# Optimization experiments

Measured on AMD Instinct MI355X. Metric: run time of the kernel, lower is better.

Reference implementation:

```python
import jax, jax.numpy as jnp
import numpy as np

B, S = 2, 2048
DIM_IN, DIM_OUT, NUM_HEADS, DIM_QK = 1024, 128, 16, 128


def setup_inputs() -> dict:
    key = jax.random.key(0)
    k0, k1, k2, k3 = jax.random.split(key, 4)
    x = jax.random.normal(k0, (B, S, DIM_IN), jnp.float32)
    mask = jax.random.bernoulli(k1, 0.1, (B, S))  # True = masked-out token
    # xavier-normal-ish scales (exact init values are irrelevant for correctness)
    std_in = float(np.sqrt(2.0 / (NUM_HEADS * DIM_QK + DIM_IN * DIM_QK)))
    proj_in = jax.random.normal(k2, (DIM_IN, NUM_HEADS, 2 * DIM_QK + DIM_OUT), jnp.float32) * std_in
    v_bias = jnp.zeros((NUM_HEADS, DIM_OUT), jnp.float32)
    std_out = float(np.sqrt(2.0 / (DIM_OUT * DIM_OUT + NUM_HEADS * DIM_OUT)))
    proj_out = jax.random.normal(k3, (NUM_HEADS, DIM_OUT, DIM_OUT), jnp.float32) * std_out
    proj_out_bias = jnp.zeros((DIM_OUT,), jnp.float32)
    return {"x": x, "mask": mask, "proj_in": proj_in, "v_bias": v_bias,
            "proj_out": proj_out, "proj_out_bias": proj_out_bias}


def _rotary(t):
    # t: [z, s, h, d]; GPT-NeoX style rotary as in the torch Rotary module
    d = t.shape[-1]
    half = -(-d // 2)  # ceil(d/2), matches torch.arange(0,-1,-2/d)
    freq_half = 10000.0 ** (jnp.arange(half, dtype=jnp.float32) * (-2.0 / d))
    freq = jnp.concatenate([freq_half, freq_half[: half - d % 2]])  # length d
    pos = jnp.arange(t.shape[1], dtype=jnp.float32)
    ang = pos[:, None] * freq[None, :]             # [s, d]
    cos = jnp.cos(ang)[None, :, None, :]
    sin = jnp.sin(ang)[None, :, None, :]
    x1, x2 = jnp.split(t, 2, axis=-1)
    rot = jnp.concatenate([-x2, x1], axis=-1)
    return t * cos + rot * sin


def _inf_cube(t):
    return t ** 3


def reference(x, mask, proj_in, v_bias, proj_out, proj_out_bias):
    qkv = jnp.einsum('zki,iho->zkho', x, proj_in)
    q, k, v = jnp.split(qkv, [DIM_QK, 2 * DIM_QK], axis=-1)
    q = _rotary(q)
    k = _rotary(k)
    scores = jnp.einsum('zqha,zkha->zqkh', q, k) / jnp.sqrt(jnp.float32(DIM_QK))
    # dual mask: row (query) OR column (key) masked -> -inf
    m = jnp.logical_or(mask[:, :, None, None], mask[:, None, :, None])  # [z,q,k,1]
    scores = jnp.where(m, -jnp.inf, scores)
    attn = jnp.nan_to_num(jax.nn.softmax(scores, axis=2))  # softmax over k; nan rows -> 0
    o = jnp.einsum('zqkh,zkhx->zqhx', attn, v + v_bias[None, None])
    out = jnp.einsum('zqhx,hxy->zqy', _inf_cube(o), proj_out) + proj_out_bias[None, None]
    return _inf_cube(out)
```

## Files before the change

kernel.cpp:

```cpp
#include <hip/hip_runtime.h>
#include <math.h>

#define BZ 2
#define SQ 2048
#define DIN 1024
#define HH 16
#define NT 6144
#define MROWS 4096
#define KOUT 2048
#define KSPLIT 8

typedef unsigned short u16t;
typedef unsigned int u32t;
typedef __attribute__((ext_vector_type(8))) short bf16x8;
typedef __attribute__((ext_vector_type(4))) float f32x4;

__device__ __forceinline__ float cubef(float x) { return x * x * x; }

__device__ __forceinline__ u16t f2bf(float f) {
    u32t b = __float_as_uint(f);
    b += 0x7FFFu + ((b >> 16) & 1u);
    return (u16t)(b >> 16);
}
__device__ __forceinline__ float bf2f(u16t u) { return __uint_as_float(((u32t)u) << 16); }
__device__ __forceinline__ u32t pk2(float a, float b) {
    return (u32t)f2bf(a) | ((u32t)f2bf(b) << 16);
}

#if __has_builtin(__builtin_amdgcn_exp2f)
#define EXP2(x) __builtin_amdgcn_exp2f(x)
#else
#define EXP2(x) exp2f(x)
#endif

__device__ __forceinline__ void load_lds16(const void* g, void* l) {
    __builtin_amdgcn_global_load_lds((const __attribute__((address_space(1))) void*)g,
                                     (__attribute__((address_space(3))) void*)l, 16, 0, 0);
}

__global__ __launch_bounds__(256) void prep_all(const float* __restrict__ x,
                                                u16t* __restrict__ xb,
                                                float* __restrict__ tab,
                                                const float* __restrict__ W,
                                                u16t* __restrict__ Th) {
    __shared__ float tile[64][68];
    const int bx = blockIdx.x;
    const int t = threadIdx.x;

    if (bx < 2048) {
        const size_t idx = ((size_t)bx * 256 + t) * 8;
        float4 f0 = *(const float4*)&x[idx];
        float4 f1 = *(const float4*)&x[idx + 4];
        u32t h[4];
        h[0] = pk2(f0.x, f0.y); h[1] = pk2(f0.z, f0.w);
        h[2] = pk2(f1.x, f1.y); h[3] = pk2(f1.z, f1.w);
        *(uint4*)&xb[idx] = *(uint4*)&h[0];
    } else if (bx < 2560) {
        const int idx = (bx - 2048) * 256 + t;
        const int s = idx >> 6, d = idx & 63;
        float f = expf(-0.14391156831212788f * (float)d);
        float sn, cs;
        sincosf((float)s * f, &sn, &cs);
        ((float2*)tab)[idx] = make_float2(cs, sn);
    } else {
        const int idx = bx - 2560;
        const int n0 = (idx % 96) * 64;
        const int k0 = (idx / 96) * 64;
        {
            const int r = t >> 4, c = (t & 15) * 4;
            #pragma unroll
            for (int p = 0; p < 4; p++) {
                float4 v = *(const float4*)&W[(size_t)(k0 + r + p * 16) * NT + n0 + c];
                *(float4*)&tile[r + p * 16][c] = v;
            }
        }
        __syncthreads();
        const int nr = t >> 2;
        const int kc = (t & 3) * 16;
        u32t hi[8];
        #pragma unroll
        for (int j = 0; j < 8; j++)
            hi[j] = pk2(tile[kc + 2 * j][nr], tile[kc + 2 * j + 1][nr]);
        size_t ob = (size_t)(n0 + nr) * DIN + k0 + kc;
        *(uint4*)&Th[ob]     = *(uint4*)&hi[0];
        *(uint4*)&Th[ob + 8] = *(uint4*)&hi[4];
    }
}

__global__ __launch_bounds__(256) void transpose_w2(const float* __restrict__ W,
                                                    u16t* __restrict__ Th) {
    __shared__ float tile[64][68];
    const int n0 = blockIdx.x * 64;
    const int k0 = blockIdx.y * 64;
    const int t = threadIdx.x;
    {
        const int r = t >> 4, c = (t & 15) * 4;
        #pragma unroll
        for (int p = 0; p < 4; p++) {
            float4 v = *(const float4*)&W[(size_t)(k0 + r + p * 16) * 128 + n0 + c];
            *(float4*)&tile[r + p * 16][c] = v;
        }
    }
    __syncthreads();
    const int nr = t >> 2;
    const int kc = (t & 3) * 16;
    u32t hi[8];
    #pragma unroll
    for (int j = 0; j < 8; j++)
        hi[j] = pk2(tile[kc + 2 * j][nr], tile[kc + 2 * j + 1][nr]);
    size_t ob = (size_t)(n0 + nr) * KOUT + k0 + kc;
    *(uint4*)&Th[ob]     = *(uint4*)&hi[0];
    *(uint4*)&Th[ob + 8] = *(uint4*)&hi[4];
}

#define QSC 0.12751744f

__global__ __launch_bounds__(256) void gemm_qkv11(const u16t* __restrict__ Ah,
                                                  const u16t* __restrict__ Bh,
                                                  const float* __restrict__ vb,
                                                  const float* __restrict__ ropetab,
                                                  u16t* __restrict__ QB,
                                                  u16t* __restrict__ KB,
                                                  u16t* __restrict__ VTh) {
    __shared__ __align__(16) u16t smem[17408];

    const int t = threadIdx.x;
    const int lane = t & 63, wid = t >> 6;
    const int quad = lane >> 4, l15 = lane & 15;
    const int wm = (wid & 1) * 64;
    const int wn = (wid >> 1) * 64;

    const int f = blockIdx.y * 48 + blockIdx.x;
    const int L = (f & 7) * 192 + (f >> 3);
    const int rect = L / 48, rrem = L - rect * 48;
    const int tileI = (rect & 7) * 6 + rrem % 6;
    const int rowIdx = (rect >> 3) * 8 + rrem / 6;
    const int h = tileI / 3, t3 = tileI - h * 3;
    const int colBase = tileI * 128;
    const int rowBase = rowIdx * 128;
    const int sm = t & 127;
    const int skh = t >> 7;

    f32x4 acc[4][4];
    #pragma unroll
    for (int i = 0; i < 4; i++)
        #pragma unroll
        for (int j = 0; j < 4; j++) acc[i][j] = (f32x4){0.f, 0.f, 0.f, 0.f};

    const u16t* aPtr = Ah + (size_t)(rowBase + sm) * DIN + skh * 16;
    const u16t* bPtr = Bh + (size_t)(colBase + sm) * DIN + skh * 16;
    const int swoff = skh * 2048 + sm * 8;

    uint4 a0 = *(const uint4*)(aPtr);
    uint4 a1 = *(const uint4*)(aPtr + 8);
    uint4 b0 = *(const uint4*)(bPtr);
    uint4 b1 = *(const uint4*)(bPtr + 8);

    for (int it = 0; it < 32; it++) {
        const int buf = it & 1;
        const int ab = buf * 4096, bb_ = 8192 + buf * 4096;
        *(uint4*)(&smem[ab + swoff])         = a0;
        *(uint4*)(&smem[ab + swoff + 1024])  = a1;
        *(uint4*)(&smem[bb_ + swoff])        = b0;
        *(uint4*)(&smem[bb_ + swoff + 1024]) = b1;
        __syncthreads();
        {
            const int k0 = (it < 31) ? (it + 1) * 32 : it * 32;
            a0 = *(const uint4*)(aPtr + k0);
            a1 = *(const uint4*)(aPtr + k0 + 8);
            b0 = *(const uint4*)(bPtr + k0);
            b1 = *(const uint4*)(bPtr + k0 + 8);
        }
        bf16x8 ah[4], bh[4];
        #pragma unroll
        for (int mt = 0; mt < 4; mt++)
            ah[mt] = *(const bf16x8*)&smem[ab + quad * 1024 + (wm + mt * 16 + l15) * 8];
        #pragma unroll
        for (int nt = 0; nt < 4; nt++)
            bh[nt] = *(const bf16x8*)&smem[bb_ + quad * 1024 + (wn + nt * 16 + l15) * 8];
        #pragma unroll
        for (int mt = 0; mt < 4; mt++)
            #pragma unroll
            for (int nt = 0; nt < 4; nt++)
                acc[mt][nt] = __builtin_amdgcn_mfma_f32_16x16x32_bf16(ah[mt], bh[nt], acc[mt][nt], 0, 0, 0);
    }
    __syncthreads();

    const int z = rowBase >> 11;
    const int s0local = rowBase & 2047;
    const size_t zh = (size_t)(z * 16 + h);
    u16t* tl = smem;

    if (t3 == 2) {
        #pragma unroll
        for (int nt = 0; nt < 4; nt++) {
            float bbv = vb[h * 128 + wn + nt * 16 + l15];
            #pragma unroll
            for (int mt = 0; mt < 4; mt++)
                #pragma unroll
                for (int r = 0; r < 4; r++)
                    tl[(wm + mt * 16 + quad * 4 + r) * 136 + wn + nt * 16 + l15] =
                        f2bf(acc[mt][nt][r] + bbv);
        }
    } else {
        #pragma unroll
        for (int nt = 0; nt < 4; nt++)
            #pragma unroll
            for (int mt = 0; mt < 4; mt++)
                #pragma unroll
                for (int r = 0; r < 4; r++)
                    tl[(wm + mt * 16 + quad * 4 + r) * 136 + wn + nt * 16 + l15] =
                        f2bf(acc[mt][nt][r]);
    }
    __syncthreads();

    if (t3 != 2) {
        u16t* dstQK = (t3 ? KB : QB) + zh * 262144;
        const float sc = t3 ? 1.0f : QSC;
        const int rr = t >> 2;
        const int ch = (t & 3) << 4;
        #pragma unroll
        for (int half = 0; half < 2; half++) {
            const int row = rr + half * 64;
            const int s = s0local + row;
            const u16t* trow = &tl[row * 136];
            uint4 X1  = *(const uint4*)&trow[ch];
            uint4 X1b = *(const uint4*)&trow[ch + 8];
            uint4 X2  = *(const uint4*)&trow[ch + 64];
            uint4 X2b = *(const uint4*)&trow[ch + 72];
            u32t A_[8] = {X1.x, X1.y, X1.z, X1.w, X1b.x, X1b.y, X1b.z, X1b.w};
            u32t B_[8] = {X2.x, X2.y, X2.z, X2.w, X2b.x, X2b.y, X2b.z, X2b.w};
            u32t OA[8], OB[8];
            const float4* tb = (const float4*)&ropetab[(size_t)s * 128 + ch * 2];
            #pragma unroll
            for (int p = 0; p < 8; p++) {
                float4 tt = tb[p];
                float cs0 = tt.x * sc, sn0 = tt.y * sc;
                float cs1 = tt.z * sc, sn1 = tt.w * sc;
                float x1a = bf2f((u16t)(A_[p] & 0xFFFFu)), x1b = bf2f((u16t)(A_[p] >> 16));
                float x2a = bf2f((u16t)(B_[p] & 0xFFFFu)), x2b = bf2f((u16t)(B_[p] >> 16));
                OA[p] = pk2(x1a * cs0 - x2a * sn0, x1b * cs1 - x2b * sn1);
                OB[p] = pk2(x2a * cs0 + x1a * sn0, x2b * cs1 + x1b * sn1);
            }
            u16t* d0 = dstQK + (size_t)s * 128 + ch;
            *(uint4*)d0        = make_uint4(OA[0], OA[1], OA[2], OA[3]);
            *(uint4*)(d0 + 8)  = make_uint4(OA[4], OA[5], OA[6], OA[7]);
            *(uint4*)(d0 + 64) = make_uint4(OB[0], OB[1], OB[2], OB[3]);
            *(uint4*)(d0 + 72) = make_uint4(OB[4], OB[5], OB[6], OB[7]);
        }
    } else {
        u16t* dstV = VTh + zh * 262144 + (size_t)(s0local >> 5) * 4096;
        const int d = t & 127;
        const int g0 = t >> 7;
        #pragma unroll
        for (int gg = 0; gg < 2; gg++) {
            const int g = g0 + 2 * gg;
            const u16t* col = &tl[(g * 32) * 136 + d];
            u32t H[16];
            #pragma unroll
            for (int m = 0; m < 16; m++) {
                u32t lo = col[m * 136];
                u32t hi = col[(m + 16) * 136];
                H[m] = lo | (hi << 16);
            }
            u16t* dv = dstV + (size_t)g * 4096 + d * 32;
            *(uint4*)&dv[0]  = *(uint4*)&H[0];
            *(uint4*)&dv[8]  = *(uint4*)&H[4];
            *(uint4*)&dv[16] = *(uint4*)&H[8];
            *(uint4*)&dv[24] = *(uint4*)&H[12];
        }
    }
}

__global__ __launch_bounds__(256, 2) void attn_kernel13(const u16t* __restrict__ QB,
                                                        const u16t* __restrict__ KB,
                                                        const u16t* __restrict__ VTh,
                                                        const int* __restrict__ mask,
                                                        u16t* __restrict__ O3b) {
    const int blk = blockIdx.x;
    const int xcd = blk & 7, loc = blk >> 3;
    const int zhl = xcd * 4 + (loc >> 4);
    const int qt = loc & 15;
    const int z = zhl >> 4, h = zhl & 15;
    const int t  = threadIdx.x;
    const int lane = t & 63, wid = t >> 6;
    const int quad = lane >> 4, l15 = lane & 15;

    __shared__ __align__(16) u16t ks[2][32 * 136];
    __shared__ __align__(16) u16t vth[2][128 * 40];
    __shared__ __align__(16) u16t wlb[128 * 40];

    const int q0 = qt * 128;
    const u16t* qb  = QB  + (size_t)zhl * 262144;
    const u16t* kb  = KB  + (size_t)zhl * 262144;
    const u16t* vhg = VTh + (size_t)zhl * 262144;
    const int mb = z * SQ;

    bf16x8 qf[2][4];
    #pragma unroll
    for (int i = 0; i < 2; i++)
        #pragma unroll
        for (int kk = 0; kk < 4; kk++)
            qf[i][kk] = *(const bf16x8*)(qb + (size_t)(q0 + 16 * (2 * wid + i) + l15) * 128 + kk * 32 + quad * 8);

    int4 qm4[2];
    #pragma unroll
    for (int i = 0; i < 2; i++)
        qm4[i] = *(const int4*)&mask[mb + q0 + 16 * (2 * wid + i) + 4 * quad];
    const int qmr[2][4] = {{qm4[0].x, qm4[0].y, qm4[0].z, qm4[0].w},
                           {qm4[1].x, qm4[1].y, qm4[1].z, qm4[1].w}};
    int rowoff[2];
    #pragma unroll
    for (int i = 0; i < 2; i++) rowoff[i] = (16 * (2 * wid + i) + 4 * quad) * 40;

    const int srow = t >> 3, sco = (t & 7) * 16;
    const int sdd = t >> 1, sk0 = (t & 1) * 16;

    uint4 ka, kb2, va, vb2;
    {
        ka  = *(const uint4*)(kb + t * 16);
        kb2 = *(const uint4*)(kb + t * 16 + 8);
        va  = *(const uint4*)(vhg + t * 16);
        vb2 = *(const uint4*)(vhg + t * 16 + 8);
    }

    f32x4 acc[2][8];
    #pragma unroll
    for (int i = 0; i < 2; i++)
        #pragma unroll
        for (int d = 0; d < 8; d++) acc[i][d] = (f32x4){0.f, 0.f, 0.f, 0.f};
    float dsum[2][4] = {{0.f, 0.f, 0.f, 0.f}, {0.f, 0.f, 0.f, 0.f}};

    for (int it = 0; it < 64; it++) {
        const int buf = it & 1;
        *(uint4*)&ks[buf][srow * 136 + sco]     = ka;
        *(uint4*)&ks[buf][srow * 136 + sco + 8] = kb2;
        *(uint4*)&vth[buf][sdd * 40 + sk0]      = va;
        *(uint4*)&vth[buf][sdd * 40 + sk0 + 8]  = vb2;

        __syncthreads();

        {
            const int ktn = (it < 63) ? (it + 1) * 32 : it * 32;
            const u16t* src = kb + (size_t)ktn * 128 + t * 16;
            ka  = *(const uint4*)(src);
            kb2 = *(const uint4*)(src + 8);
            const u16t* srch = vhg + (size_t)(ktn >> 5) * 4096 + t * 16;
            va  = *(const uint4*)(srch);
            vb2 = *(const uint4*)(srch + 8);
        }

        const int colm0 = mask[mb + it * 32 + l15];
        const int colm1 = mask[mb + it * 32 + 16 + l15];

        f32x4 s4[2][2];
        #pragma unroll
        for (int i = 0; i < 2; i++)
            #pragma unroll
            for (int n = 0; n < 2; n++) s4[i][n] = (f32x4){0.f, 0.f, 0.f, 0.f};
        __builtin_amdgcn_s_setprio(1);
        #pragma unroll
        for (int kk = 0; kk < 4; kk++) {
            bf16x8 kf0 = *(const bf16x8*)&ks[buf][l15 * 136 + kk * 32 + quad * 8];
            bf16x8 kf1 = *(const bf16x8*)&ks[buf][(16 + l15) * 136 + kk * 32 + quad * 8];
            s4[0][0] = __builtin_amdgcn_mfma_f32_16x16x32_bf16(qf[0][kk], kf0, s4[0][0], 0, 0, 0);
            s4[0][1] = __builtin_amdgcn_mfma_f32_16x16x32_bf16(qf[0][kk], kf1, s4[0][1], 0, 0, 0);
            s4[1][0] = __builtin_amdgcn_mfma_f32_16x16x32_bf16(qf[1][kk], kf0, s4[1][0], 0, 0, 0);
            s4[1][1] = __builtin_amdgcn_mfma_f32_16x16x32_bf16(qf[1][kk], kf1, s4[1][1], 0, 0, 0);
        }
        __builtin_amdgcn_s_setprio(0);
        {
            #pragma unroll
            for (int i = 0; i < 2; i++)
                #pragma unroll
                for (int r = 0; r < 4; r++) {
                    float w0 = colm0 ? 0.f : EXP2(s4[i][0][r]);
                    float w1 = colm1 ? 0.f : EXP2(s4[i][1][r]);
                    dsum[i][r] += w0 + w1;
                    u32t pkw;
                    asm("v_cvt_pk_bf16_f32 %0, %1, %2" : "=v"(pkw) : "v"(w0), "v"(w1));
                    *(u32t*)&wlb[rowoff[i] + r * 40 + 2 * l15] = pkw;
                }
        }
        bf16x8 pa[2];
        #pragma unroll
        for (int i = 0; i < 2; i++)
            pa[i] = *(const bf16x8*)&wlb[(16 * (2 * wid + i) + l15) * 40 + quad * 8];
        __builtin_amdgcn_s_setprio(1);
        #pragma unroll
        for (int dt = 0; dt < 8; dt++) {
            bf16x8 vh = *(const bf16x8*)&vth[buf][(16 * dt + l15) * 40 + quad * 8];
            acc[0][dt] = __builtin_amdgcn_mfma_f32_16x16x32_bf16(pa[0], vh, acc[0][dt], 0, 0, 0);
            acc[1][dt] = __builtin_amdgcn_mfma_f32_16x16x32_bf16(pa[1], vh, acc[1][dt], 0, 0, 0);
        }
        __builtin_amdgcn_s_setprio(0);
    }

    #pragma unroll
    for (int i = 0; i < 2; i++)
        #pragma unroll
        for (int r = 0; r < 4; r++) {
            float v = dsum[i][r];
            v += __shfl_xor(v, 1);
            v += __shfl_xor(v, 2);
            v += __shfl_xor(v, 4);
            v += __shfl_xor(v, 8);
            dsum[i][r] = v;
        }

    #pragma unroll
    for (int i = 0; i < 2; i++)
        #pragma unroll
        for (int r = 0; r < 4; r++) {
            int row = 16 * (2 * wid + i) + 4 * quad + r;
            float inv = (qmr[i][r] || !(dsum[i][r] > 0.f)) ? 0.f : 1.f / dsum[i][r];
            u16t* dst = O3b + (size_t)(z * SQ + q0 + row) * KOUT + h * 128;
            #pragma unroll
            for (int dt = 0; dt < 8; dt++)
                dst[16 * dt + l15] = f2bf(cubef(acc[i][dt][r] * inv));
        }
}

#define GQ_WAITBAR(N) do {                                                 \
    asm volatile("s_waitcnt vmcnt(" #N ")" ::: "memory");                  \
    __builtin_amdgcn_s_barrier();                                          \
    __builtin_amdgcn_sched_barrier(0);                                     \
} while (0)

#define GQ_STAGE(TI) do {                                                  \
    const int _k0 = (TI) * 32;                                             \
    const int _bb = ((TI) & 3) * 8192;                                     \
    load_lds16(aPtr + _k0,     &smem[_bb + wbase]);                        \
    load_lds16(aPtr + _k0 + 8, &smem[_bb + wbase + 1024]);                 \
    load_lds16(bPtr + _k0,     &smem[_bb + 4096 + wbase]);                 \
    load_lds16(bPtr + _k0 + 8, &smem[_bb + 4096 + wbase + 1024]);          \
} while (0)

#define GQ_COMPUTE(TI) do {                                                \
    const int _bb = ((TI) & 3) * 8192;                                     \
    bf16x8 ah[4], bh[4];                                                   \
    _Pragma("unroll")                                                      \
    for (int mt = 0; mt < 4; mt++)                                         \
        ah[mt] = *(const bf16x8*)&smem[_bb + quad * 1024 + (wm + mt * 16 + l15) * 8]; \
    _Pragma("unroll")                                                      \
    for (int nt = 0; nt < 4; nt++)                                         \
        bh[nt] = *(const bf16x8*)&smem[_bb + 4096 + quad * 1024 + (wn + nt * 16 + l15) * 8]; \
    _Pragma("unroll")                                                      \
    for (int mt = 0; mt < 4; mt++)                                         \
        _Pragma("unroll")                                                  \
        for (int nt = 0; nt < 4; nt++)                                     \
            acc[mt][nt] = __builtin_amdgcn_mfma_f32_16x16x32_bf16(ah[mt], bh[nt], acc[mt][nt], 0, 0, 0); \
} while (0)

__global__ __launch_bounds__(256, 2) void final_gemm4(const u16t* __restrict__ Ab,
                                                      const u16t* __restrict__ Bh,
                                                      float* __restrict__ part) {
    __shared__ __align__(16) u16t smem[32768];

    const int t = threadIdx.x;
    const int lane = t & 63, wid = t >> 6;
    const int quad = lane >> 4, l15 = lane & 15;
    const int wm = (wid & 1) * 64;
    const int wn = (wid >> 1) * 64;
    const int rowBase = blockIdx.x * 128;
    const int kBase   = blockIdx.y * (KOUT / KSPLIT);
    const int sm = t & 127;
    const int skh = t >> 7;

    f32x4 acc[4][4];
    #pragma unroll
    for (int i = 0; i < 4; i++)
        #pragma unroll
        for (int j = 0; j < 4; j++) acc[i][j] = (f32x4){0.f, 0.f, 0.f, 0.f};

    const u16t* aPtr = Ab + (size_t)(rowBase + sm) * KOUT + kBase + skh * 16;
    const u16t* bPtr = Bh + (size_t)sm * KOUT + kBase + skh * 16;
    const int wbase = (wid >> 1) * 2048 + (wid & 1) * 512;

    GQ_STAGE(0);
    GQ_STAGE(1);
    for (int i = 0; i < 6; i++) {
        GQ_STAGE(i + 2);
        GQ_WAITBAR(8);
        GQ_COMPUTE(i);
    }
    GQ_WAITBAR(4);
    GQ_COMPUTE(6);
    GQ_WAITBAR(0);
    GQ_COMPUTE(7);

    float* pbase = part + (size_t)blockIdx.y * ((size_t)MROWS * 128);
    #pragma unroll
    for (int mt = 0; mt < 4; mt++)
        #pragma unroll
        for (int nt = 0; nt < 4; nt++) {
            int col = wn + nt * 16 + l15;
            #pragma unroll
            for (int r = 0; r < 4; r++) {
                int row = rowBase + wm + mt * 16 + quad * 4 + r;
                pbase[(size_t)row * 128 + col] = acc[mt][nt][r];
            }
        }
}

__global__ __launch_bounds__(256) void reduce_bias_cube(const float* __restrict__ part,
                                                        const float* __restrict__ bias,
                                                        float* __restrict__ out) {
    const int idx = (blockIdx.x * 256 + threadIdx.x) * 4;
    float4 s = {0.f, 0.f, 0.f, 0.f};
    #pragma unroll
    for (int p = 0; p < KSPLIT; p++) {
        float4 v = *(const float4*)&part[(size_t)p * ((size_t)MROWS * 128) + idx];
        s.x += v.x; s.y += v.y; s.z += v.z; s.w += v.w;
    }
    float4 b = *(const float4*)&bias[idx & 127];
    float4 r;
    r.x = cubef(s.x + b.x);
    r.y = cubef(s.y + b.y);
    r.z = cubef(s.z + b.z);
    r.w = cubef(s.w + b.w);
    *(float4*)&out[idx] = r;
}

extern "C" void kernel_launch(void* const* d_in, const int* in_sizes, int n_in,
                              void* d_out, int out_size, void* d_ws, size_t ws_size,
                              hipStream_t stream) {
    const float* x        = (const float*)d_in[0];
    const int*   mask     = (const int*)d_in[1];
    const float* proj_in  = (const float*)d_in[2];
    const float* v_bias   = (const float*)d_in[3];
    const float* proj_out = (const float*)d_in[4];
    const float* po_bias  = (const float*)d_in[5];
    float* out = (float*)d_out;

    u16t* QB  = (u16t*)d_ws;
    u16t* KB  = QB + (size_t)8388608;
    u16t* VTh = KB + (size_t)8388608;
    u16t* xb  = VTh + (size_t)8388608;
    u16t* O3b = xb + (size_t)4194304;
    u16t* pTh = O3b;
    float* ropetab = (float*)(O3b + (size_t)6291456);
    u16t* WTh = QB;
    float* partials = (float*)(WTh + (size_t)128 * KOUT);

    prep_all<<<2048 + 512 + 1536, 256, 0, stream>>>(x, xb, ropetab, proj_in, pTh);
    gemm_qkv11<<<dim3(48, 32), 256, 0, stream>>>(xb, pTh, v_bias, ropetab, QB, KB, VTh);
    attn_kernel13<<<BZ * HH * (SQ / 128), 256, 0, stream>>>(QB, KB, VTh, mask, O3b);
    transpose_w2<<<dim3(2, KOUT / 64), 256, 0, stream>>>(proj_out, WTh);
    final_gemm4<<<dim3(MROWS / 128, KSPLIT), 256, 0, stream>>>(O3b, WTh, partials);
    reduce_bias_cube<<<(MROWS * 128) / (256 * 4), 256, 0, stream>>>(partials, po_bias, out);
}
```

Measured before the change: 295.2 us.

## Pipeline QKV GEMM with triple-buffered direct global-to-LDS loads

Replaces the register-staged double-buffered main loop of the QKV projection GEMM with a three-stage pipeline that uses direct global-to-LDS loads (load_lds16), vmcnt waits and one barrier per iteration. Two k-tiles are kept in flight while the current one is computed, which hides global load latency and drops the register round trip for staging. The cost is more LDS (48KB), which may lower occupancy. Correctness depends on the wbase layout matching what the compute reads and on each thread's async loads landing in order.

```diff
diff --git a/kernel.cpp b/kernel.cpp
--- a/kernel.cpp
+++ b/kernel.cpp
@@ -115,14 +115,45 @@
 
 #define QSC 0.12751744f
 
-__global__ __launch_bounds__(256) void gemm_qkv11(const u16t* __restrict__ Ah,
+#define GQ3_WAITBAR(N) do {                                                \
+    asm volatile("s_waitcnt vmcnt(" #N ")" ::: "memory");                  \
+    __builtin_amdgcn_s_barrier();                                          \
+    __builtin_amdgcn_sched_barrier(0);                                     \
+} while (0)
+
+#define GQ3_STAGE(TI) do {                                                 \
+    const int _k0 = (TI) * 32;                                             \
+    const int _bb = ((TI) % 3) * 8192;                                     \
+    load_lds16(aPtr + _k0,     &smem[_bb + wbase]);                        \
+    load_lds16(aPtr + _k0 + 8, &smem[_bb + wbase + 1024]);                 \
+    load_lds16(bPtr + _k0,     &smem[_bb + 4096 + wbase]);                 \
+    load_lds16(bPtr + _k0 + 8, &smem[_bb + 4096 + wbase + 1024]);          \
+} while (0)
+
+#define GQ3_COMPUTE(TI) do {                                               \
+    const int _bb = ((TI) % 3) * 8192;                                     \
+    bf16x8 ah[4], bh[4];                                                   \
+    _Pragma("unroll")                                                      \
+    for (int mt = 0; mt < 4; mt++)                                         \
+        ah[mt] = *(const bf16x8*)&smem[_bb + quad * 1024 + (wm + mt * 16 + l15) * 8]; \
+    _Pragma("unroll")                                                      \
+    for (int nt = 0; nt < 4; nt++)                                         \
+        bh[nt] = *(const bf16x8*)&smem[_bb + 4096 + quad * 1024 + (wn + nt * 16 + l15) * 8]; \
+    _Pragma("unroll")                                                      \
+    for (int mt = 0; mt < 4; mt++)                                         \
+        _Pragma("unroll")                                                  \
+        for (int nt = 0; nt < 4; nt++)                                     \
+            acc[mt][nt] = __builtin_amdgcn_mfma_f32_16x16x32_bf16(ah[mt], bh[nt], acc[mt][nt], 0, 0, 0); \
+} while (0)
+
+__global__ __launch_bounds__(256) void gemm_qkv12(const u16t* __restrict__ Ah,
                                                   const u16t* __restrict__ Bh,
                                                   const float* __restrict__ vb,
                                                   const float* __restrict__ ropetab,
                                                   u16t* __restrict__ QB,
                                                   u16t* __restrict__ KB,
                                                   u16t* __restrict__ VTh) {
-    __shared__ __align__(16) u16t smem[17408];
+    __shared__ __align__(16) u16t smem[24576];
 
     const int t = threadIdx.x;
     const int lane = t & 63, wid = t >> 6;
@@ -149,41 +180,19 @@
 
     const u16t* aPtr = Ah + (size_t)(rowBase + sm) * DIN + skh * 16;
     const u16t* bPtr = Bh + (size_t)(colBase + sm) * DIN + skh * 16;
-    const int swoff = skh * 2048 + sm * 8;
-
-    uint4 a0 = *(const uint4*)(aPtr);
-    uint4 a1 = *(const uint4*)(aPtr + 8);
-    uint4 b0 = *(const uint4*)(bPtr);
-    uint4 b1 = *(const uint4*)(bPtr + 8);
-
-    for (int it = 0; it < 32; it++) {
-        const int buf = it & 1;
-        const int ab = buf * 4096, bb_ = 8192 + buf * 4096;
-        *(uint4*)(&smem[ab + swoff])         = a0;
-        *(uint4*)(&smem[ab + swoff + 1024])  = a1;
-        *(uint4*)(&smem[bb_ + swoff])        = b0;
-        *(uint4*)(&smem[bb_ + swoff + 1024]) = b1;
-        __syncthreads();
-        {
-            const int k0 = (it < 31) ? (it + 1) * 32 : it * 32;
-            a0 = *(const uint4*)(aPtr + k0);
-            a1 = *(const uint4*)(aPtr + k0 + 8);
-            b0 = *(const uint4*)(bPtr + k0);
-            b1 = *(const uint4*)(bPtr + k0 + 8);
-        }
-        bf16x8 ah[4], bh[4];
-        #pragma unroll
-        for (int mt = 0; mt < 4; mt++)
-            ah[mt] = *(const bf16x8*)&smem[ab + quad * 1024 + (wm + mt * 16 + l15) * 8];
-        #pragma unroll
-        for (int nt = 0; nt < 4; nt++)
-            bh[nt] = *(const bf16x8*)&smem[bb_ + quad * 1024 + (wn + nt * 16 + l15) * 8];
-        #pragma unroll
-        for (int mt = 0; mt < 4; mt++)
-            #pragma unroll
-            for (int nt = 0; nt < 4; nt++)
-                acc[mt][nt] = __builtin_amdgcn_mfma_f32_16x16x32_bf16(ah[mt], bh[nt], acc[mt][nt], 0, 0, 0);
-    }
+    const int wbase = (wid >> 1) * 2048 + (wid & 1) * 512;
+
+    GQ3_STAGE(0);
+    GQ3_STAGE(1);
+    for (int i = 0; i < 30; i++) {
+        GQ3_WAITBAR(4);
+        GQ3_STAGE(i + 2);
+        GQ3_COMPUTE(i);
+    }
+    GQ3_WAITBAR(4);
+    GQ3_COMPUTE(30);
+    GQ3_WAITBAR(0);
+    GQ3_COMPUTE(31);
     __syncthreads();
 
     const int z = rowBase >> 11;
@@ -544,7 +553,7 @@
     float* partials = (float*)(WTh + (size_t)128 * KOUT);
 
     prep_all<<<2048 + 512 + 1536, 256, 0, stream>>>(x, xb, ropetab, proj_in, pTh);
-    gemm_qkv11<<<dim3(48, 32), 256, 0, stream>>>(xb, pTh, v_bias, ropetab, QB, KB, VTh);
+    gemm_qkv12<<<dim3(48, 32), 256, 0, stream>>>(xb, pTh, v_bias, ropetab, QB, KB, VTh);
     attn_kernel13<<<BZ * HH * (SQ / 128), 256, 0, stream>>>(QB, KB, VTh, mask, O3b);
     transpose_w2<<<dim3(2, KOUT / 64), 256, 0, stream>>>(proj_out, WTh);
     final_gemm4<<<dim3(MROWS / 128, KSPLIT), 256, 0, stream>>>(O3b, WTh, partials);
```

After: 298.7 us, median of 2. About the same (+1.2%).

## Pipeline QKV GEMM with direct-to-LDS loads in a 4-stage ring buffer

Applied to the files above, without the earlier changes.

Replaces the QKV projection GEMM's register-staged double buffer with direct global-to-LDS loads into a 4-slot ring, prefetching two K-steps ahead with vmcnt-based waits and one barrier per step. It also raises MFMA wave priority during compute through the shared macros and sets launch bounds to two blocks per CU. The aim is to hide global load latency and cut per-iteration synchronisation. In exchange LDS use grows to 64KB per block, which may limit occupancy, and the fixed wait counts must match the issued loads exactly.

```diff
diff --git a/kernel.cpp b/kernel.cpp
--- a/kernel.cpp
+++ b/kernel.cpp
@@ -115,14 +115,47 @@
 
 #define QSC 0.12751744f
 
-__global__ __launch_bounds__(256) void gemm_qkv11(const u16t* __restrict__ Ah,
-                                                  const u16t* __restrict__ Bh,
-                                                  const float* __restrict__ vb,
-                                                  const float* __restrict__ ropetab,
-                                                  u16t* __restrict__ QB,
-                                                  u16t* __restrict__ KB,
-                                                  u16t* __restrict__ VTh) {
-    __shared__ __align__(16) u16t smem[17408];
+#define GQ_WAITBAR(N) do {                                                 \
+    asm volatile("s_waitcnt vmcnt(" #N ")" ::: "memory");                  \
+    __builtin_amdgcn_s_barrier();                                          \
+    __builtin_amdgcn_sched_barrier(0);                                     \
+} while (0)
+
+#define GQ_STAGE(TI) do {                                                  \
+    const int _k0 = (TI) * 32;                                             \
+    const int _bb = ((TI) & 3) * 8192;                                     \
+    load_lds16(aPtr + _k0,     &smem[_bb + wbase]);                        \
+    load_lds16(aPtr + _k0 + 8, &smem[_bb + wbase + 1024]);                 \
+    load_lds16(bPtr + _k0,     &smem[_bb + 4096 + wbase]);                 \
+    load_lds16(bPtr + _k0 + 8, &smem[_bb + 4096 + wbase + 1024]);          \
+} while (0)
+
+#define GQ_COMPUTE(TI) do {                                                \
+    const int _bb = ((TI) & 3) * 8192;                                     \
+    bf16x8 ah[4], bh[4];                                                   \
+    _Pragma("unroll")                                                      \
+    for (int mt = 0; mt < 4; mt++)                                         \
+        ah[mt] = *(const bf16x8*)&smem[_bb + quad * 1024 + (wm + mt * 16 + l15) * 8]; \
+    _Pragma("unroll")                                                      \
+    for (int nt = 0; nt < 4; nt++)                                         \
+        bh[nt] = *(const bf16x8*)&smem[_bb + 4096 + quad * 1024 + (wn + nt * 16 + l15) * 8]; \
+    __builtin_amdgcn_s_setprio(1);                                         \
+    _Pragma("unroll")                                                      \
+    for (int mt = 0; mt < 4; mt++)                                         \
+        _Pragma("unroll")                                                  \
+        for (int nt = 0; nt < 4; nt++)                                     \
+            acc[mt][nt] = __builtin_amdgcn_mfma_f32_16x16x32_bf16(ah[mt], bh[nt], acc[mt][nt], 0, 0, 0); \
+    __builtin_amdgcn_s_setprio(0);                                         \
+} while (0)
+
+__global__ __launch_bounds__(256, 2) void gemm_qkv6(const u16t* __restrict__ Ah,
+                                                    const u16t* __restrict__ Bh,
+                                                    const float* __restrict__ vb,
+                                                    const float* __restrict__ ropetab,
+                                                    u16t* __restrict__ QB,
+                                                    u16t* __restrict__ KB,
+                                                    u16t* __restrict__ VTh) {
+    __shared__ __align__(16) u16t smem[32768];
 
     const int t = threadIdx.x;
     const int lane = t & 63, wid = t >> 6;
@@ -149,41 +182,19 @@
 
     const u16t* aPtr = Ah + (size_t)(rowBase + sm) * DIN + skh * 16;
     const u16t* bPtr = Bh + (size_t)(colBase + sm) * DIN + skh * 16;
-    const int swoff = skh * 2048 + sm * 8;
-
-    uint4 a0 = *(const uint4*)(aPtr);
-    uint4 a1 = *(const uint4*)(aPtr + 8);
-    uint4 b0 = *(const uint4*)(bPtr);
-    uint4 b1 = *(const uint4*)(bPtr + 8);
-
-    for (int it = 0; it < 32; it++) {
-        const int buf = it & 1;
-        const int ab = buf * 4096, bb_ = 8192 + buf * 4096;
-        *(uint4*)(&smem[ab + swoff])         = a0;
-        *(uint4*)(&smem[ab + swoff + 1024])  = a1;
-        *(uint4*)(&smem[bb_ + swoff])        = b0;
-        *(uint4*)(&smem[bb_ + swoff + 1024]) = b1;
-        __syncthreads();
-        {
-            const int k0 = (it < 31) ? (it + 1) * 32 : it * 32;
-            a0 = *(const uint4*)(aPtr + k0);
-            a1 = *(const uint4*)(aPtr + k0 + 8);
-            b0 = *(const uint4*)(bPtr + k0);
-            b1 = *(const uint4*)(bPtr + k0 + 8);
-        }
-        bf16x8 ah[4], bh[4];
-        #pragma unroll
-        for (int mt = 0; mt < 4; mt++)
-            ah[mt] = *(const bf16x8*)&smem[ab + quad * 1024 + (wm + mt * 16 + l15) * 8];
-        #pragma unroll
-        for (int nt = 0; nt < 4; nt++)
-            bh[nt] = *(const bf16x8*)&smem[bb_ + quad * 1024 + (wn + nt * 16 + l15) * 8];
-        #pragma unroll
-        for (int mt = 0; mt < 4; mt++)
-            #pragma unroll
-            for (int nt = 0; nt < 4; nt++)
-                acc[mt][nt] = __builtin_amdgcn_mfma_f32_16x16x32_bf16(ah[mt], bh[nt], acc[mt][nt], 0, 0, 0);
-    }
+    const int wbase = (wid >> 1) * 2048 + (wid & 1) * 512;
+
+    GQ_STAGE(0);
+    GQ_STAGE(1);
+    for (int i = 0; i < 30; i++) {
+        GQ_STAGE(i + 2);
+        GQ_WAITBAR(8);
+        GQ_COMPUTE(i);
+    }
+    GQ_WAITBAR(4);
+    GQ_COMPUTE(30);
+    GQ_WAITBAR(0);
+    GQ_COMPUTE(31);
     __syncthreads();
 
     const int z = rowBase >> 11;
@@ -421,37 +432,6 @@
         }
 }
 
-#define GQ_WAITBAR(N) do {                                                 \
-    asm volatile("s_waitcnt vmcnt(" #N ")" ::: "memory");                  \
-    __builtin_amdgcn_s_barrier();                                          \
-    __builtin_amdgcn_sched_barrier(0);                                     \
-} while (0)
-
-#define GQ_STAGE(TI) do {                                                  \
-    const int _k0 = (TI) * 32;                                             \
-    const int _bb = ((TI) & 3) * 8192;                                     \
-    load_lds16(aPtr + _k0,     &smem[_bb + wbase]);                        \
-    load_lds16(aPtr + _k0 + 8, &smem[_bb + wbase + 1024]);                 \
-    load_lds16(bPtr + _k0,     &smem[_bb + 4096 + wbase]);                 \
-    load_lds16(bPtr + _k0 + 8, &smem[_bb + 4096 + wbase + 1024]);          \
-} while (0)
-
-#define GQ_COMPUTE(TI) do {                                                \
-    const int _bb = ((TI) & 3) * 8192;                                     \
-    bf16x8 ah[4], bh[4];                                                   \
-    _Pragma("unroll")                                                      \
-    for (int mt = 0; mt < 4; mt++)                                         \
-        ah[mt] = *(const bf16x8*)&smem[_bb + quad * 1024 + (wm + mt * 16 + l15) * 8]; \
-    _Pragma("unroll")                                                      \
-    for (int nt = 0; nt < 4; nt++)                                         \
-        bh[nt] = *(const bf16x8*)&smem[_bb + 4096 + quad * 1024 + (wn + nt * 16 + l15) * 8]; \
-    _Pragma("unroll")                                                      \
-    for (int mt = 0; mt < 4; mt++)                                         \
-        _Pragma("unroll")                                                  \
-        for (int nt = 0; nt < 4; nt++)                                     \
-            acc[mt][nt] = __builtin_amdgcn_mfma_f32_16x16x32_bf16(ah[mt], bh[nt], acc[mt][nt], 0, 0, 0); \
-} while (0)
-
 __global__ __launch_bounds__(256, 2) void final_gemm4(const u16t* __restrict__ Ab,
                                                       const u16t* __restrict__ Bh,
                                                       float* __restrict__ part) {
@@ -544,7 +524,7 @@
     float* partials = (float*)(WTh + (size_t)128 * KOUT);
 
     prep_all<<<2048 + 512 + 1536, 256, 0, stream>>>(x, xb, ropetab, proj_in, pTh);
-    gemm_qkv11<<<dim3(48, 32), 256, 0, stream>>>(xb, pTh, v_bias, ropetab, QB, KB, VTh);
+    gemm_qkv6<<<dim3(48, 32), 256, 0, stream>>>(xb, pTh, v_bias, ropetab, QB, KB, VTh);
     attn_kernel13<<<BZ * HH * (SQ / 128), 256, 0, stream>>>(QB, KB, VTh, mask, O3b);
     transpose_w2<<<dim3(2, KOUT / 64), 256, 0, stream>>>(proj_out, WTh);
     final_gemm4<<<dim3(MROWS / 128, KSPLIT), 256, 0, stream>>>(O3b, WTh, partials);
```

Measured after the change: 295.6 us. About the same (+0.1%).
